# Kernel optimization log

Measured on AMD Instinct MI355X. Metric: run time of the kernel, lower is better.

The kernel has to match this reference:

```python
import jax, jax.numpy as jnp
import numpy as np

N_NODES = 100_000
N_EDGES = 1_250_000
IN_FEATS, N_HIDDEN, N_CLASSES = 64, 64, 32


def setup_inputs() -> dict:
    key = jax.random.key(0)
    ks = jax.random.split(key, 8)
    x = jax.random.normal(ks[0], (N_NODES, IN_FEATS), dtype=jnp.float32)
    src = jax.random.randint(ks[1], (N_EDGES,), 0, N_NODES, dtype=jnp.int64)
    dst = jax.random.randint(ks[2], (N_EDGES,), 0, N_NODES, dtype=jnp.int64)
    s1 = 1.0 / np.sqrt(IN_FEATS)
    s2 = 1.0 / np.sqrt(N_HIDDEN)
    W_self1 = jax.random.normal(ks[3], (IN_FEATS, N_HIDDEN), dtype=jnp.float32) * s1
    W_neigh1 = jax.random.normal(ks[4], (IN_FEATS, N_HIDDEN), dtype=jnp.float32) * s1
    b1 = jnp.zeros((N_HIDDEN,), dtype=jnp.float32)
    W_self2 = jax.random.normal(ks[5], (N_HIDDEN, N_CLASSES), dtype=jnp.float32) * s2
    W_neigh2 = jax.random.normal(ks[6], (N_HIDDEN, N_CLASSES), dtype=jnp.float32) * s2
    b2 = jnp.zeros((N_CLASSES,), dtype=jnp.float32)
    return dict(x=x, src=src, dst=dst, W_self1=W_self1, W_neigh1=W_neigh1, b1=b1,
                W_self2=W_self2, W_neigh2=W_neigh2, b2=b2)


def _sage_conv(h, src, dst, W_self, W_neigh, b):
    # mean aggregation over in-neighbors: gather src feats, segment-sum by dst
    n = h.shape[0]
    msg = h[src]  # [E, d] -- dominant memory traffic
    agg = jax.ops.segment_sum(msg, dst, num_segments=n)
    deg = jax.ops.segment_sum(jnp.ones_like(dst, dtype=h.dtype), dst, num_segments=n)
    h_neigh = agg / jnp.maximum(deg, 1.0)[:, None]  # zero-degree nodes get 0 (DGL behavior)
    return h @ W_self + h_neigh @ W_neigh + b


def reference(x, src, dst, W_self1, W_neigh1, b1, W_self2, W_neigh2, b2):
    h = _sage_conv(x, src, dst, W_self1, W_neigh1, b1)
    h = jax.nn.relu(h)
    # dropout(p=0.5) is identity in eval mode
    return _sage_conv(h, src, dst, W_self2, W_neigh2, b2)
```

## Files before the change

### kernel.cpp

```cpp
#include <hip/hip_runtime.h>
#include <hip/hip_bf16.h>


#define NF 64
#define BW 256
#define BSH 8
#define MAXB 512
#define CAPMAX 8192
#define P1_CHUNK 2048
#define H1S 68

typedef __attribute__((ext_vector_type(8))) short short8;
typedef __attribute__((ext_vector_type(8))) unsigned short ushort8v;
typedef __attribute__((ext_vector_type(4))) float floatx4;

__device__ __forceinline__ short bf16hi(float v) {
    __hip_bfloat16 h = __float2bfloat16(v);
    return *(short*)&h;
}
__device__ __forceinline__ float bf2f(short s) {
    __hip_bfloat16 h = *(__hip_bfloat16*)&s;
    return __bfloat162float(h);
}
__device__ __forceinline__ float bits2f(unsigned short u) {
    unsigned int x = ((unsigned int)u) << 16;
    union { unsigned int i; float f; } c; c.i = x; return c.f;
}


__global__ __launch_bounds__(256) void prep_kernel(
        int* __restrict__ gcursor,
        const float* __restrict__ Ws1, const float* __restrict__ Wn1,
        const float* __restrict__ Ws2, const float* __restrict__ Wn2,
        unsigned short* __restrict__ w1p, unsigned short* __restrict__ w2p) {
    const int tid = threadIdx.x;
    if (blockIdx.x == 0) {
        for (int i = tid; i < MAXB; i += 256) gcursor[i] = 0;
        return;
    }
    const int part = blockIdx.x - 1;
    for (int i = tid; i < 32 * 64; i += 256) {
        int n = part * 32 + (i >> 6), k = i & 63;
        float v = (n < 64) ? Ws1[k * 64 + n] : Wn1[k * 64 + (n - 64)];
        short hv = bf16hi(v);
        w1p[n * 64 + k] = (unsigned short)hv;
        w1p[8192 + n * 64 + k] = (unsigned short)bf16hi(v - bf2f(hv));
    }
    for (int i = tid; i < 16 * 64; i += 256) {
        int n = part * 16 + (i >> 6), k = i & 63;
        float v = (n < 32) ? Ws2[k * 32 + n] : Wn2[k * 32 + (n - 32)];
        short hv = bf16hi(v);
        w2p[n * 64 + k] = (unsigned short)hv;
        w2p[4096 + n * 64 + k] = (unsigned short)bf16hi(v - bf2f(hv));
    }
}


__global__ __launch_bounds__(256) void p1_dense1_kernel(
        const int* __restrict__ src, const int* __restrict__ dst,
        int* __restrict__ gcursor, unsigned* __restrict__ bucket,
        int E, int nbuckets, int dblocks,
        const float* __restrict__ X,
        const unsigned short* __restrict__ w1p,
        const float* __restrict__ bias,
        float* __restrict__ outA,
        unsigned short* __restrict__ outB,
        int N) {
    __shared__ int smem_i[2 * MAXB];
    const int tid = threadIdx.x;

    if ((int)blockIdx.x >= dblocks) {
        int* cnt   = smem_i;
        int* cbase = smem_i + MAXB;
        const int bid = blockIdx.x - dblocks;
        const int beg = bid * P1_CHUNK;
        const int end = min(E, beg + P1_CHUNK);
        for (int i = tid; i < nbuckets; i += 256) cnt[i] = 0;
        __syncthreads();
        for (int e = beg + tid; e < end; e += 256)
            atomicAdd(&cnt[dst[e] >> BSH], 1);
        __syncthreads();
        for (int i = tid; i < nbuckets; i += 256) {
            int c = cnt[i];
            cbase[i] = c ? atomicAdd(&gcursor[i], c) : 0;
            cnt[i] = 0;
        }
        __syncthreads();
        for (int e = beg + tid; e < end; e += 256) {
            int d = dst[e];
            int r = d >> BSH;
            int p = cbase[r] + atomicAdd(&cnt[r], 1);
            if (p < CAPMAX)
                bucket[(size_t)r * CAPMAX + p] = ((unsigned)src[e] << BSH) | (unsigned)(d & (BW - 1));
        }
        return;
    }

    constexpr int NT = 8, NSELF = 4;
    const int lane = tid & 63;
    const int wid  = tid >> 6;
    const int m = lane & 15, quad = lane >> 4;
    const int rowblk = blockIdx.x * 128 + wid * 32;

    floatx4 acc[2][NT];
    #pragma unroll
    for (int rt = 0; rt < 2; ++rt)
        #pragma unroll
        for (int t = 0; t < NT; ++t) acc[rt][t] = (floatx4)(0.f);

    short8 ah[2][2], al[2][2];
    #pragma unroll
    for (int rt = 0; rt < 2; ++rt) {
        int r = rowblk + rt * 16 + m;
        if (r >= N) r = N - 1;
        const float* xp = X + (size_t)r * 64 + quad * 8;
        #pragma unroll
        for (int h = 0; h < 2; ++h) {
            floatx4 f0 = *(const floatx4*)(xp + h * 32);
            floatx4 f1 = *(const floatx4*)(xp + h * 32 + 4);
            short8 hi, lo;
            #pragma unroll
            for (int j = 0; j < 4; ++j) {
                short hv = bf16hi(f0[j]);
                hi[j] = hv; lo[j] = bf16hi(f0[j] - bf2f(hv));
                short hv2 = bf16hi(f1[j]);
                hi[4 + j] = hv2; lo[4 + j] = bf16hi(f1[j] - bf2f(hv2));
            }
            ah[rt][h] = hi; al[rt][h] = lo;
        }
    }

    #pragma unroll
    for (int t = 0; t < NT; ++t) {
        int n = t * 16 + m;
        const unsigned short* ph = w1p + n * 64 + quad * 8;
        const unsigned short* pl = ph + 8192;
        #pragma unroll
        for (int h = 0; h < 2; ++h) {
            short8 bh = *(const short8*)(ph + h * 32);
            short8 bl = *(const short8*)(pl + h * 32);
            #pragma unroll
            for (int rt = 0; rt < 2; ++rt) {
                acc[rt][t] = __builtin_amdgcn_mfma_f32_16x16x32_bf16(ah[rt][h], bh, acc[rt][t], 0, 0, 0);
                acc[rt][t] = __builtin_amdgcn_mfma_f32_16x16x32_bf16(al[rt][h], bh, acc[rt][t], 0, 0, 0);
                acc[rt][t] = __builtin_amdgcn_mfma_f32_16x16x32_bf16(ah[rt][h], bl, acc[rt][t], 0, 0, 0);
            }
        }
    }

    #pragma unroll
    for (int rt = 0; rt < 2; ++rt) {
        #pragma unroll
        for (int t = 0; t < NT; ++t) {
            #pragma unroll
            for (int r4 = 0; r4 < 4; ++r4) {
                int row = rowblk + rt * 16 + quad * 4 + r4;
                if (row < N) {
                    if (t < NSELF) {
                        int col = t * 16 + m;
                        outA[(size_t)row * 64 + col] = acc[rt][t][r4] + bias[col];
                    } else {
                        int col = (t - NSELF) * 16 + m;
                        outB[(size_t)row * 64 + col] = (unsigned short)bf16hi(acc[rt][t][r4]);
                    }
                }
            }
        }
    }
}


__global__ __launch_bounds__(256) void p2_csr_kernel(const unsigned* __restrict__ bucket,
                                                     const int* __restrict__ gcursor,
                                                     int* __restrict__ row_start,
                                                     int* __restrict__ csr_src,
                                                     int N, int nbuckets) {
    __shared__ unsigned stage[CAPMAX];
    __shared__ int cnt[BW];
    __shared__ int excl[BW];
    const int r = blockIdx.x;
    const int tid = threadIdx.x;

    int partial = 0;
    for (int i = tid; i < r; i += 256) partial += min(gcursor[i], CAPMAX);
    excl[tid] = partial;
    __syncthreads();
    for (int off = 128; off > 0; off >>= 1) {
        if (tid < off) excl[tid] += excl[tid + off];
        __syncthreads();
    }
    const int base = excl[0];
    const int sz = min(gcursor[r], CAPMAX);
    const unsigned* bsrc = bucket + (size_t)r * CAPMAX;
    __syncthreads();

    cnt[tid] = 0;
    __syncthreads();
    for (int i = tid; i < sz; i += 256) {
        unsigned v = bsrc[i];
        stage[i] = v;
        atomicAdd(&cnt[v & (BW - 1)], 1);
    }
    __syncthreads();
    excl[tid] = cnt[tid];
    __syncthreads();
    for (int off = 1; off < BW; off <<= 1) {
        int v0 = (tid >= off) ? excl[tid - off] : 0;
        __syncthreads();
        excl[tid] += v0;
        __syncthreads();
    }
    int node = r * BW + tid;
    if (node < N) row_start[node] = base + excl[tid] - cnt[tid];
    if (r == nbuckets - 1 && tid == 0) row_start[N] = base + sz;
    __syncthreads();
    cnt[tid] = excl[tid] - cnt[tid];
    __syncthreads();
    for (int i = tid; i < sz; i += 256) {
        unsigned v = stage[i];
        int p = atomicAdd(&cnt[v & (BW - 1)], 1);
        csr_src[base + p] = (int)(v >> BSH);
    }
}


__global__ __launch_bounds__(256) void agg64_d2_kernel(
        const unsigned short* __restrict__ t1n,
        const float* __restrict__ xs,
        const int* __restrict__ row_start,
        const int* __restrict__ csr_src,
        const unsigned short* __restrict__ w2p,
        const float* __restrict__ b2,
        float* __restrict__ outD,
        unsigned short* __restrict__ t2n,
        int N, int E) {
    __shared__ float h1s[16][H1S];
    const int tid = threadIdx.x;
    const int lane = tid & 63;
    const int wid  = tid >> 6;
    const int half = lane >> 5;
    const int g = (lane >> 3) & 3;
    const int c = lane & 7;
    const int nbase = blockIdx.x * 16;

    const int ln0 = wid * 4 + half;
    const int ln1 = ln0 + 2;
    const int n0 = nbase + ln0, n1 = nbase + ln1;
    int beg0 = 0, end0 = 0, beg1 = 0, end1 = 0;
    if (n0 < N) { beg0 = row_start[n0]; end0 = row_start[n0 + 1]; }
    if (n1 < N) { beg1 = row_start[n1]; end1 = row_start[n1 + 1]; }

    float a0[8] = {0.f, 0.f, 0.f, 0.f, 0.f, 0.f, 0.f, 0.f};
    float a1[8] = {0.f, 0.f, 0.f, 0.f, 0.f, 0.f, 0.f, 0.f};
    int j0 = beg0 + g, j1 = beg1 + g;
    const int Em1 = E - 1;
    while ((j0 < end0) || (j1 < end1)) {
        int s0 = csr_src[min(j0, Em1)];
        int s1 = csr_src[min(j0 + 4, Em1)];
        int s2 = csr_src[min(j1, Em1)];
        int s3 = csr_src[min(j1 + 4, Em1)];
        s0 = ((unsigned)s0 < (unsigned)N) ? s0 : 0;
        s1 = ((unsigned)s1 < (unsigned)N) ? s1 : 0;
        s2 = ((unsigned)s2 < (unsigned)N) ? s2 : 0;
        s3 = ((unsigned)s3 < (unsigned)N) ? s3 : 0;
        ushort8v u0 = *(const ushort8v*)(t1n + (size_t)s0 * 64 + c * 8);
        ushort8v u1 = *(const ushort8v*)(t1n + (size_t)s1 * 64 + c * 8);
        ushort8v u2 = *(const ushort8v*)(t1n + (size_t)s2 * 64 + c * 8);
        ushort8v u3 = *(const ushort8v*)(t1n + (size_t)s3 * 64 + c * 8);
        const bool c00 = j0 < end0, c01 = j0 + 4 < end0;
        const bool c10 = j1 < end1, c11 = j1 + 4 < end1;
        #pragma unroll
        for (int i = 0; i < 8; ++i) {
            a0[i] += (c00 ? bits2f(u0[i]) : 0.f) + (c01 ? bits2f(u1[i]) : 0.f);
            a1[i] += (c10 ? bits2f(u2[i]) : 0.f) + (c11 ? bits2f(u3[i]) : 0.f);
        }
        j0 += 8; j1 += 8;
    }

    const int m = lane & 15, quad = lane >> 4;
    const int coln = wid * 16 + m;
    const unsigned short* pb = w2p + coln * 64 + quad * 8;
    short8 bhf0 = *(const short8*)(pb);
    short8 bhf1 = *(const short8*)(pb + 32);
    short8 blf0 = *(const short8*)(pb + 4096);
    short8 blf1 = *(const short8*)(pb + 4096 + 32);

    floatx4 x00 = (floatx4)(0.f), x01 = (floatx4)(0.f);
    floatx4 x10 = (floatx4)(0.f), x11 = (floatx4)(0.f);
    if (g == 0) {
        if (n0 < N) {
            const float* p = xs + (size_t)n0 * 64 + c * 8;
            x00 = *(const floatx4*)p; x01 = *(const floatx4*)(p + 4);
        }
        if (n1 < N) {
            const float* p = xs + (size_t)n1 * 64 + c * 8;
            x10 = *(const floatx4*)p; x11 = *(const floatx4*)(p + 4);
        }
    }

    #pragma unroll
    for (int i = 0; i < 8; ++i) {
        float v = a0[i];
        v += __shfl_xor(v, 8);
        v += __shfl_xor(v, 16);
        a0[i] = v;
        float w = a1[i];
        w += __shfl_xor(w, 8);
        w += __shfl_xor(w, 16);
        a1[i] = w;
    }
    if (g == 0) {
        floatx4 h0, h1v;
        if (n0 < N) {
            float invd = 1.0f / fmaxf((float)(end0 - beg0), 1.0f);
            #pragma unroll
            for (int i = 0; i < 4; ++i) {
                h0[i]  = fmaxf(x00[i] + a0[i] * invd, 0.f);
                h1v[i] = fmaxf(x01[i] + a0[4 + i] * invd, 0.f);
            }
        } else { h0 = (floatx4)(0.f); h1v = (floatx4)(0.f); }
        *(floatx4*)&h1s[ln0][c * 8]     = h0;
        *(floatx4*)&h1s[ln0][c * 8 + 4] = h1v;
        if (n1 < N) {
            float invd = 1.0f / fmaxf((float)(end1 - beg1), 1.0f);
            #pragma unroll
            for (int i = 0; i < 4; ++i) {
                h0[i]  = fmaxf(x10[i] + a1[i] * invd, 0.f);
                h1v[i] = fmaxf(x11[i] + a1[4 + i] * invd, 0.f);
            }
        } else { h0 = (floatx4)(0.f); h1v = (floatx4)(0.f); }
        *(floatx4*)&h1s[ln1][c * 8]     = h0;
        *(floatx4*)&h1s[ln1][c * 8 + 4] = h1v;
    }
    __syncthreads();

    short8 ah[2], al[2];
    #pragma unroll
    for (int h = 0; h < 2; ++h) {
        const float* hp = &h1s[m][quad * 8 + h * 32];
        floatx4 f0 = *(const floatx4*)hp;
        floatx4 f1 = *(const floatx4*)(hp + 4);
        short8 hi, lo;
        #pragma unroll
        for (int j = 0; j < 4; ++j) {
            short hv = bf16hi(f0[j]);
            hi[j] = hv; lo[j] = bf16hi(f0[j] - bf2f(hv));
            short hv2 = bf16hi(f1[j]);
            hi[4 + j] = hv2; lo[4 + j] = bf16hi(f1[j] - bf2f(hv2));
        }
        ah[h] = hi; al[h] = lo;
    }
    floatx4 acc2 = (floatx4)(0.f);
    acc2 = __builtin_amdgcn_mfma_f32_16x16x32_bf16(ah[0], bhf0, acc2, 0, 0, 0);
    acc2 = __builtin_amdgcn_mfma_f32_16x16x32_bf16(al[0], bhf0, acc2, 0, 0, 0);
    acc2 = __builtin_amdgcn_mfma_f32_16x16x32_bf16(ah[0], blf0, acc2, 0, 0, 0);
    acc2 = __builtin_amdgcn_mfma_f32_16x16x32_bf16(ah[1], bhf1, acc2, 0, 0, 0);
    acc2 = __builtin_amdgcn_mfma_f32_16x16x32_bf16(al[1], bhf1, acc2, 0, 0, 0);
    acc2 = __builtin_amdgcn_mfma_f32_16x16x32_bf16(ah[1], blf1, acc2, 0, 0, 0);
    #pragma unroll
    for (int r4 = 0; r4 < 4; ++r4) {
        int node = nbase + quad * 4 + r4;
        if (node < N) {
            if (coln < 32) outD[(size_t)node * 32 + coln] = acc2[r4] + b2[coln];
            else t2n[(size_t)node * 32 + (coln - 32)] = (unsigned short)bf16hi(acc2[r4]);
        }
    }
}


__global__ __launch_bounds__(256) void agg32_kernel(float* io,
                                                    const unsigned short* __restrict__ t2n,
                                                    const int* __restrict__ row_start,
                                                    const int* __restrict__ csr_src, int N) {
    int n = (blockIdx.x * blockDim.x + threadIdx.x) >> 6;
    if (n >= N) return;
    int lane = threadIdx.x & 63;
    int g = lane >> 2, c = lane & 3;
    int beg = row_start[n], end = row_start[n + 1];
    floatx4 s0v = (floatx4)(0.f), s1v = (floatx4)(0.f);
    size_t o = (size_t)n * 32 + c * 8;
    if (g == 0) {
        s0v = *(const floatx4*)(io + o);
        s1v = *(const floatx4*)(io + o + 4);
    }
    float acc[8] = {0.f, 0.f, 0.f, 0.f, 0.f, 0.f, 0.f, 0.f};
    for (int j = beg + g; j < end; j += 32) {
        int j2 = j + 16;
        int s0 = csr_src[j];
        ushort8v u0 = *(const ushort8v*)(t2n + (size_t)s0 * 32 + c * 8);
        if (j2 < end) {
            int s1 = csr_src[j2];
            ushort8v u1 = *(const ushort8v*)(t2n + (size_t)s1 * 32 + c * 8);
            #pragma unroll
            for (int i = 0; i < 8; ++i) acc[i] += bits2f(u0[i]) + bits2f(u1[i]);
        } else {
            #pragma unroll
            for (int i = 0; i < 8; ++i) acc[i] += bits2f(u0[i]);
        }
    }
    #pragma unroll
    for (int i = 0; i < 8; ++i) {
        float v = acc[i];
        v += __shfl_xor(v, 4);
        v += __shfl_xor(v, 8);
        v += __shfl_xor(v, 16);
        v += __shfl_xor(v, 32);
        acc[i] = v;
    }
    if (g == 0) {
        float inv = 1.0f / fmaxf((float)(end - beg), 1.0f);
        floatx4 r0, r1;
        #pragma unroll
        for (int i = 0; i < 4; ++i) {
            r0[i] = s0v[i] + acc[i] * inv;
            r1[i] = s1v[i] + acc[4 + i] * inv;
        }
        *(floatx4*)(io + o) = r0;
        *(floatx4*)(io + o + 4) = r1;
    }
}


__global__ __launch_bounds__(256) void deg_kernel(const int* __restrict__ dst,
                                                  float* __restrict__ deg, int E) {
    int e = blockIdx.x * blockDim.x + threadIdx.x;
    if (e < E) atomicAdd(&deg[dst[e]], 1.0f);
}

__global__ __launch_bounds__(256) void agg_atomic_kernel(const float* __restrict__ feats,
                                                         const int* __restrict__ src,
                                                         const int* __restrict__ dst,
                                                         float* __restrict__ agg, int E) {
    int tid = blockIdx.x * blockDim.x + threadIdx.x;
    if (tid >= E * NF) return;
    int e = tid >> 6, f = tid & 63;
    atomicAdd(&agg[(size_t)dst[e] * NF + f], feats[(size_t)src[e] * NF + f]);
}

__global__ __launch_bounds__(256) void layer1_fb_kernel(const float* __restrict__ x,
                                                        const float* __restrict__ agg,
                                                        const float* __restrict__ deg,
                                                        const float* __restrict__ Wself,
                                                        const float* __restrict__ Wneigh,
                                                        const float* __restrict__ b,
                                                        float* __restrict__ h1, int N) {
    int tid = blockIdx.x * blockDim.x + threadIdx.x;
    if (tid >= N * NF) return;
    int n = tid >> 6, c = tid & 63;
    float inv = 1.0f / fmaxf(deg[n], 1.0f);
    const float* xrow = x + (size_t)n * NF;
    const float* arow = agg + (size_t)n * NF;
    float acc = b[c];
    #pragma unroll
    for (int k = 0; k < NF; ++k) {
        acc += xrow[k] * Wself[k * NF + c];
        acc += (arow[k] * inv) * Wneigh[k * NF + c];
    }
    h1[tid] = fmaxf(acc, 0.f);
}

__global__ __launch_bounds__(256) void layer2_fb_kernel(const float* __restrict__ h1,
                                                        const float* __restrict__ agg,
                                                        const float* __restrict__ deg,
                                                        const float* __restrict__ Wself,
                                                        const float* __restrict__ Wneigh,
                                                        const float* __restrict__ b,
                                                        float* __restrict__ out, int N) {
    int tid = blockIdx.x * blockDim.x + threadIdx.x;
    if (tid >= N * 32) return;
    int n = tid >> 5, c = tid & 31;
    float inv = 1.0f / fmaxf(deg[n], 1.0f);
    const float* hrow = h1 + (size_t)n * NF;
    const float* arow = agg + (size_t)n * NF;
    float acc = b[c];
    #pragma unroll
    for (int k = 0; k < NF; ++k) {
        acc += hrow[k] * Wself[k * 32 + c];
        acc += (arow[k] * inv) * Wneigh[k * 32 + c];
    }
    out[tid] = acc;
}


extern "C" void kernel_launch(void* const* d_in, const int* in_sizes, int n_in,
                              void* d_out, int out_size, void* d_ws, size_t ws_size,
                              hipStream_t stream) {
    const float* x        = (const float*)d_in[0];
    const int*   src      = (const int*)d_in[1];
    const int*   dst      = (const int*)d_in[2];
    const float* W_self1  = (const float*)d_in[3];
    const float* W_neigh1 = (const float*)d_in[4];
    const float* b1       = (const float*)d_in[5];
    const float* W_self2  = (const float*)d_in[6];
    const float* W_neigh2 = (const float*)d_in[7];
    const float* b2       = (const float*)d_in[8];
    float* out = (float*)d_out;

    const int N = in_sizes[0] / NF;
    const int E = in_sizes[1];
    const int nbuckets = (N + BW - 1) / BW;

    const size_t rsPad = ((size_t)N + 8) & ~7ull;
    int* gcursor   = (int*)d_ws;
    unsigned short* w2p = (unsigned short*)(gcursor + MAXB);
    unsigned short* w1p = w2p + 8192;
    int* row_start = (int*)(w1p + 16384);
    int* csr_src   = row_start + rsPad;
    uintptr_t pa = (uintptr_t)(csr_src + (((size_t)E + 7) & ~7ull));
    pa = (pa + 127) & ~(uintptr_t)127;
    float* bufA = (float*)pa;
    unsigned* bucket = (unsigned*)bufA;
    unsigned short* t1n = (unsigned short*)(bufA + (size_t)N * NF);
    unsigned short* t2n = t1n + (size_t)N * NF;
    size_t need = (size_t)((char*)(t2n + (size_t)N * 32) - (char*)d_ws);

    bool fast = ws_size >= need
             && nbuckets <= MAXB
             && (size_t)nbuckets * CAPMAX <= (size_t)N * NF
             && (size_t)E * 2 / (size_t)nbuckets <= CAPMAX
             && N < (1 << 24)
             && out_size >= N * 32;

    if (fast) {
        prep_kernel<<<5, 256, 0, stream>>>(gcursor, W_self1, W_neigh1,
                                           W_self2, W_neigh2, w1p, w2p);
        int dblocks  = (N + 127) / 128;
        int p1blocks = (E + P1_CHUNK - 1) / P1_CHUNK;
        unsigned* bucket2 = (unsigned*)(t2n + (((size_t)N * 32 + 63) & ~63ull));
        size_t need2 = (size_t)((char*)(bucket2 + (size_t)nbuckets * CAPMAX) - (char*)d_ws);
        if (ws_size >= need2) {
            p1_dense1_kernel<<<dblocks + p1blocks, 256, 0, stream>>>(
                src, dst, gcursor, bucket2, E, nbuckets, dblocks,
                x, w1p, b1, bufA, t1n, N);
            p2_csr_kernel<<<nbuckets, 256, 0, stream>>>(bucket2, gcursor,
                                                        row_start, csr_src, N, nbuckets);
        } else {
            p1_dense1_kernel<<<p1blocks, 256, 0, stream>>>(
                src, dst, gcursor, bucket, E, nbuckets, 0,
                x, w1p, b1, bufA, t1n, N);
            p2_csr_kernel<<<nbuckets, 256, 0, stream>>>(bucket, gcursor,
                                                        row_start, csr_src, N, nbuckets);
            p1_dense1_kernel<<<dblocks, 256, 0, stream>>>(
                src, dst, gcursor, bucket, E, nbuckets, dblocks,
                x, w1p, b1, bufA, t1n, N);
        }
        agg64_d2_kernel<<<(N + 15) / 16, 256, 0, stream>>>(
            t1n, bufA, row_start, csr_src, w2p, b2, out, t2n, N, E);
        agg32_kernel<<<(N * 64 + 255) / 256, 256, 0, stream>>>(out, t2n,
                                                               row_start, csr_src, N);
    } else {
        float* deg = (float*)d_ws;
        float* agg = deg + N;
        float* h1  = agg + (size_t)N * NF;
        hipMemsetAsync(deg, 0, (size_t)(N + (size_t)N * NF) * sizeof(float), stream);
        deg_kernel<<<(E + 255) / 256, 256, 0, stream>>>(dst, deg, E);
        int at = E * NF;
        agg_atomic_kernel<<<(at + 255) / 256, 256, 0, stream>>>(x, src, dst, agg, E);
        layer1_fb_kernel<<<(N * NF + 255) / 256, 256, 0, stream>>>(x, agg, deg, W_self1,
                                                                   W_neigh1, b1, h1, N);
        hipMemsetAsync(agg, 0, (size_t)N * NF * sizeof(float), stream);
        agg_atomic_kernel<<<(at + 255) / 256, 256, 0, stream>>>(h1, src, dst, agg, E);
        layer2_fb_kernel<<<(N * 32 + 255) / 256, 256, 0, stream>>>(h1, agg, deg, W_self2,
                                                                   W_neigh2, b2, out, N);
    }
}
```

Measured before the change: 213.8 us.

## Build CSR via degree histogram, prefix scan and global-atomic scatter

Replaces the two-pass bucketed CSR construction (LDS-local bucket sort into a staging buffer, then a per-bucket counting sort) with a degree histogram using global atomics, a two-kernel prefix scan to get row_start, and a direct scatter of src ids into csr_src using per-node atomic cursors. The scatter stays fused with the first dense layer kernel. This removes the bucket staging buffer and the LDS-heavy sort kernel, but adds a memset, two scan kernels, and about a million global atomics on random addresses. Edge order within a row is no longer deterministic, which can change floating-point summation order.

```diff
diff --git a/kernel.cpp b/kernel.cpp
--- a/kernel.cpp
+++ b/kernel.cpp
@@ -3,16 +3,12 @@
 
 
 #define NF 64
-#define BW 256
-#define BSH 8
-#define MAXB 512
-#define CAPMAX 8192
-#define P1_CHUNK 2048
 #define H1S 68
 
 typedef __attribute__((ext_vector_type(8))) short short8;
 typedef __attribute__((ext_vector_type(8))) unsigned short ushort8v;
 typedef __attribute__((ext_vector_type(4))) float floatx4;
+typedef __attribute__((ext_vector_type(4))) int intx4;
 
 __device__ __forceinline__ short bf16hi(float v) {
     __hip_bfloat16 h = __float2bfloat16(v);
@@ -28,71 +24,147 @@
 }
 
 
-__global__ __launch_bounds__(256) void prep_kernel(
-        int* __restrict__ gcursor,
+__global__ __launch_bounds__(256) void pack_hist_kernel(
+        const int* __restrict__ dst, int* __restrict__ deg, int E, int N,
         const float* __restrict__ Ws1, const float* __restrict__ Wn1,
         const float* __restrict__ Ws2, const float* __restrict__ Wn2,
         unsigned short* __restrict__ w1p, unsigned short* __restrict__ w2p) {
     const int tid = threadIdx.x;
-    if (blockIdx.x == 0) {
-        for (int i = tid; i < MAXB; i += 256) gcursor[i] = 0;
+    if (blockIdx.x < 4) {
+        const int part = blockIdx.x;
+        for (int i = tid; i < 32 * 64; i += 256) {
+            int n = part * 32 + (i >> 6), k = i & 63;
+            float v = (n < 64) ? Ws1[k * 64 + n] : Wn1[k * 64 + (n - 64)];
+            short hv = bf16hi(v);
+            w1p[n * 64 + k] = (unsigned short)hv;
+            w1p[8192 + n * 64 + k] = (unsigned short)bf16hi(v - bf2f(hv));
+        }
+        for (int i = tid; i < 16 * 64; i += 256) {
+            int n = part * 16 + (i >> 6), k = i & 63;
+            float v = (n < 32) ? Ws2[k * 32 + n] : Wn2[k * 32 + (n - 32)];
+            short hv = bf16hi(v);
+            w2p[n * 64 + k] = (unsigned short)hv;
+            w2p[4096 + n * 64 + k] = (unsigned short)bf16hi(v - bf2f(hv));
+        }
         return;
     }
-    const int part = blockIdx.x - 1;
-    for (int i = tid; i < 32 * 64; i += 256) {
-        int n = part * 32 + (i >> 6), k = i & 63;
-        float v = (n < 64) ? Ws1[k * 64 + n] : Wn1[k * 64 + (n - 64)];
-        short hv = bf16hi(v);
-        w1p[n * 64 + k] = (unsigned short)hv;
-        w1p[8192 + n * 64 + k] = (unsigned short)bf16hi(v - bf2f(hv));
-    }
-    for (int i = tid; i < 16 * 64; i += 256) {
-        int n = part * 16 + (i >> 6), k = i & 63;
-        float v = (n < 32) ? Ws2[k * 32 + n] : Wn2[k * 32 + (n - 32)];
-        short hv = bf16hi(v);
-        w2p[n * 64 + k] = (unsigned short)hv;
-        w2p[4096 + n * 64 + k] = (unsigned short)bf16hi(v - bf2f(hv));
-    }
-}
-
-
-__global__ __launch_bounds__(256) void p1_dense1_kernel(
+    const int base = (blockIdx.x - 4) * 1024 + tid;
+    #pragma unroll
+    for (int k = 0; k < 4; ++k) {
+        int e = base + k * 256;
+        if (e < E) {
+            int d = dst[e];
+            if ((unsigned)d < (unsigned)N) atomicAdd(&deg[d], 1);
+        }
+    }
+}
+
+
+__global__ __launch_bounds__(256) void scan1_kernel(const int* __restrict__ deg,
+                                                    int* __restrict__ blocksum, int N) {
+    __shared__ int red[256];
+    const int t = threadIdx.x;
+    const int base = blockIdx.x * 1024;
+    int s = 0;
+    #pragma unroll
+    for (int k = 0; k < 4; ++k) {
+        int n = base + t + k * 256;
+        if (n < N) s += deg[n];
+    }
+    red[t] = s;
+    __syncthreads();
+    for (int off = 128; off > 0; off >>= 1) {
+        if (t < off) red[t] += red[t + off];
+        __syncthreads();
+    }
+    if (t == 0) blocksum[blockIdx.x] = red[0];
+}
+
+
+__global__ __launch_bounds__(256) void scan3_kernel(const int* __restrict__ deg,
+                                                    const int* __restrict__ blocksum,
+                                                    int* __restrict__ row_start,
+                                                    int* __restrict__ cursor,
+                                                    int N, int NB, int E) {
+    __shared__ int lds[256];
+    const int b = blockIdx.x, t = threadIdx.x;
+    int partial = 0;
+    for (int i = t; i < b; i += 256) partial += blocksum[i];
+    lds[t] = partial;
+    __syncthreads();
+    for (int off = 128; off > 0; off >>= 1) {
+        if (t < off) lds[t] += lds[t + off];
+        __syncthreads();
+    }
+    const int boff = lds[0];
+    __syncthreads();
+
+    const int n0 = b * 1024 + t * 4;
+    int d0 = 0, d1 = 0, d2 = 0, d3 = 0;
+    if (n0 + 3 < N) {
+        intx4 v = *(const intx4*)(deg + n0);
+        d0 = v[0]; d1 = v[1]; d2 = v[2]; d3 = v[3];
+    } else {
+        if (n0 + 0 < N) d0 = deg[n0];
+        if (n0 + 1 < N) d1 = deg[n0 + 1];
+        if (n0 + 2 < N) d2 = deg[n0 + 2];
+        if (n0 + 3 < N) d3 = deg[n0 + 3];
+    }
+    const int tsum = d0 + d1 + d2 + d3;
+    lds[t] = tsum;
+    __syncthreads();
+    for (int off = 1; off < 256; off <<= 1) {
+        int v = (t >= off) ? lds[t - off] : 0;
+        __syncthreads();
+        lds[t] += v;
+        __syncthreads();
+    }
+    const int excl = boff + lds[t] - tsum;
+    const int r0 = excl, r1 = r0 + d0, r2 = r1 + d1, r3 = r2 + d2;
+    if (n0 + 3 < N) {
+        intx4 rv; rv[0] = r0; rv[1] = r1; rv[2] = r2; rv[3] = r3;
+        *(intx4*)(row_start + n0) = rv;
+        *(intx4*)(cursor + n0) = rv;
+    } else {
+        if (n0 + 0 < N) { row_start[n0]     = r0; cursor[n0]     = r0; }
+        if (n0 + 1 < N) { row_start[n0 + 1] = r1; cursor[n0 + 1] = r1; }
+        if (n0 + 2 < N) { row_start[n0 + 2] = r2; cursor[n0 + 2] = r2; }
+        if (n0 + 3 < N) { row_start[n0 + 3] = r3; cursor[n0 + 3] = r3; }
+    }
+    if (b == NB - 1 && t == 255) row_start[N] = E;
+}
+
+
+__global__ __launch_bounds__(256) void dense1_scatter_kernel(
         const int* __restrict__ src, const int* __restrict__ dst,
-        int* __restrict__ gcursor, unsigned* __restrict__ bucket,
-        int E, int nbuckets, int dblocks,
+        int* __restrict__ cursor, int* __restrict__ csr_src,
+        int E, int dblocks,
         const float* __restrict__ X,
         const unsigned short* __restrict__ w1p,
         const float* __restrict__ bias,
         float* __restrict__ outA,
         unsigned short* __restrict__ outB,
         int N) {
-    __shared__ int smem_i[2 * MAXB];
     const int tid = threadIdx.x;
 
     if ((int)blockIdx.x >= dblocks) {
-        int* cnt   = smem_i;
-        int* cbase = smem_i + MAXB;
-        const int bid = blockIdx.x - dblocks;
-        const int beg = bid * P1_CHUNK;
-        const int end = min(E, beg + P1_CHUNK);
-        for (int i = tid; i < nbuckets; i += 256) cnt[i] = 0;
-        __syncthreads();
-        for (int e = beg + tid; e < end; e += 256)
-            atomicAdd(&cnt[dst[e] >> BSH], 1);
-        __syncthreads();
-        for (int i = tid; i < nbuckets; i += 256) {
-            int c = cnt[i];
-            cbase[i] = c ? atomicAdd(&gcursor[i], c) : 0;
-            cnt[i] = 0;
-        }
-        __syncthreads();
-        for (int e = beg + tid; e < end; e += 256) {
-            int d = dst[e];
-            int r = d >> BSH;
-            int p = cbase[r] + atomicAdd(&cnt[r], 1);
-            if (p < CAPMAX)
-                bucket[(size_t)r * CAPMAX + p] = ((unsigned)src[e] << BSH) | (unsigned)(d & (BW - 1));
-        }
+        const int base = (blockIdx.x - dblocks) * 1024 + tid;
+        const int e0 = base, e1 = base + 256, e2 = base + 512, e3 = base + 768;
+        int d0 = 0, d1 = 0, d2 = 0, d3 = 0, s0 = 0, s1 = 0, s2 = 0, s3 = 0;
+        const bool v0 = e0 < E, v1 = e1 < E, v2 = e2 < E, v3 = e3 < E;
+        if (v0) { d0 = dst[e0]; s0 = src[e0]; }
+        if (v1) { d1 = dst[e1]; s1 = src[e1]; }
+        if (v2) { d2 = dst[e2]; s2 = src[e2]; }
+        if (v3) { d3 = dst[e3]; s3 = src[e3]; }
+        int p0 = 0, p1 = 0, p2 = 0, p3 = 0;
+        if (v0 && (unsigned)d0 < (unsigned)N) p0 = atomicAdd(&cursor[d0], 1); else p0 = -1;
+        if (v1 && (unsigned)d1 < (unsigned)N) p1 = atomicAdd(&cursor[d1], 1); else p1 = -1;
+        if (v2 && (unsigned)d2 < (unsigned)N) p2 = atomicAdd(&cursor[d2], 1); else p2 = -1;
+        if (v3 && (unsigned)d3 < (unsigned)N) p3 = atomicAdd(&cursor[d3], 1); else p3 = -1;
+        if (p0 >= 0) csr_src[p0] = s0;
+        if (p1 >= 0) csr_src[p1] = s1;
+        if (p2 >= 0) csr_src[p2] = s2;
+        if (p3 >= 0) csr_src[p3] = s3;
         return;
     }
 
@@ -166,60 +238,6 @@
                 }
             }
         }
-    }
-}
-
-
-__global__ __launch_bounds__(256) void p2_csr_kernel(const unsigned* __restrict__ bucket,
-                                                     const int* __restrict__ gcursor,
-                                                     int* __restrict__ row_start,
-                                                     int* __restrict__ csr_src,
-                                                     int N, int nbuckets) {
-    __shared__ unsigned stage[CAPMAX];
-    __shared__ int cnt[BW];
-    __shared__ int excl[BW];
-    const int r = blockIdx.x;
-    const int tid = threadIdx.x;
-
-    int partial = 0;
-    for (int i = tid; i < r; i += 256) partial += min(gcursor[i], CAPMAX);
-    excl[tid] = partial;
-    __syncthreads();
-    for (int off = 128; off > 0; off >>= 1) {
-        if (tid < off) excl[tid] += excl[tid + off];
-        __syncthreads();
-    }
-    const int base = excl[0];
-    const int sz = min(gcursor[r], CAPMAX);
-    const unsigned* bsrc = bucket + (size_t)r * CAPMAX;
-    __syncthreads();
-
-    cnt[tid] = 0;
-    __syncthreads();
-    for (int i = tid; i < sz; i += 256) {
-        unsigned v = bsrc[i];
-        stage[i] = v;
-        atomicAdd(&cnt[v & (BW - 1)], 1);
-    }
-    __syncthreads();
-    excl[tid] = cnt[tid];
-    __syncthreads();
-    for (int off = 1; off < BW; off <<= 1) {
-        int v0 = (tid >= off) ? excl[tid - off] : 0;
-        __syncthreads();
-        excl[tid] += v0;
-        __syncthreads();
-    }
-    int node = r * BW + tid;
-    if (node < N) row_start[node] = base + excl[tid] - cnt[tid];
-    if (r == nbuckets - 1 && tid == 0) row_start[N] = base + sz;
-    __syncthreads();
-    cnt[tid] = excl[tid] - cnt[tid];
-    __syncthreads();
-    for (int i = tid; i < sz; i += 256) {
-        unsigned v = stage[i];
-        int p = atomicAdd(&cnt[v & (BW - 1)], 1);
-        csr_src[base + p] = (int)(v >> BSH);
     }
 }
 
@@ -498,69 +516,55 @@
 
     const int N = in_sizes[0] / NF;
     const int E = in_sizes[1];
-    const int nbuckets = (N + BW - 1) / BW;
-
-    const size_t rsPad = ((size_t)N + 8) & ~7ull;
-    int* gcursor   = (int*)d_ws;
-    unsigned short* w2p = (unsigned short*)(gcursor + MAXB);
-    unsigned short* w1p = w2p + 8192;
-    int* row_start = (int*)(w1p + 16384);
-    int* csr_src   = row_start + rsPad;
-    uintptr_t pa = (uintptr_t)(csr_src + (((size_t)E + 7) & ~7ull));
-    pa = (pa + 127) & ~(uintptr_t)127;
-    float* bufA = (float*)pa;
-    unsigned* bucket = (unsigned*)bufA;
-    unsigned short* t1n = (unsigned short*)(bufA + (size_t)N * NF);
-    unsigned short* t2n = t1n + (size_t)N * NF;
-    size_t need = (size_t)((char*)(t2n + (size_t)N * 32) - (char*)d_ws);
+    const int NB = (N + 1023) / 1024;
+
+    uintptr_t p = (uintptr_t)d_ws;
+    auto align_up = [](uintptr_t v, uintptr_t a) { return (v + a - 1) & ~(a - 1); };
+    int* deg = (int*)p;            p += (size_t)N * 4;       p = align_up(p, 64);
+    int* cursor = (int*)p;         p += (size_t)N * 4;       p = align_up(p, 64);
+    int* row_start = (int*)p;      p += ((size_t)N + 8) * 4; p = align_up(p, 64);
+    int* blocksum = (int*)p;       p += 1024;                p = align_up(p, 64);
+    unsigned short* w2p = (unsigned short*)p; p += 8192 * 2;
+    unsigned short* w1p = (unsigned short*)p; p += 16384 * 2;
+    int* csr_src = (int*)p;        p += (size_t)E * 4;       p = align_up(p, 128);
+    float* bufA = (float*)p;       p += (size_t)N * 64 * 4;
+    unsigned short* t1n = (unsigned short*)p; p += (size_t)N * 64 * 2;
+    unsigned short* t2n = (unsigned short*)p; p += (size_t)N * 32 * 2;
+    size_t need = (size_t)(p - (uintptr_t)d_ws);
 
     bool fast = ws_size >= need
-             && nbuckets <= MAXB
-             && (size_t)nbuckets * CAPMAX <= (size_t)N * NF
-             && (size_t)E * 2 / (size_t)nbuckets <= CAPMAX
-             && N < (1 << 24)
+             && NB <= 256
+             && N >= 4
              && out_size >= N * 32;
 
     if (fast) {
-        prep_kernel<<<5, 256, 0, stream>>>(gcursor, W_self1, W_neigh1,
-                                           W_self2, W_neigh2, w1p, w2p);
-        int dblocks  = (N + 127) / 128;
-        int p1blocks = (E + P1_CHUNK - 1) / P1_CHUNK;
-        unsigned* bucket2 = (unsigned*)(t2n + (((size_t)N * 32 + 63) & ~63ull));
-        size_t need2 = (size_t)((char*)(bucket2 + (size_t)nbuckets * CAPMAX) - (char*)d_ws);
-        if (ws_size >= need2) {
-            p1_dense1_kernel<<<dblocks + p1blocks, 256, 0, stream>>>(
-                src, dst, gcursor, bucket2, E, nbuckets, dblocks,
-                x, w1p, b1, bufA, t1n, N);
-            p2_csr_kernel<<<nbuckets, 256, 0, stream>>>(bucket2, gcursor,
-                                                        row_start, csr_src, N, nbuckets);
-        } else {
-            p1_dense1_kernel<<<p1blocks, 256, 0, stream>>>(
-                src, dst, gcursor, bucket, E, nbuckets, 0,
-                x, w1p, b1, bufA, t1n, N);
-            p2_csr_kernel<<<nbuckets, 256, 0, stream>>>(bucket, gcursor,
-                                                        row_start, csr_src, N, nbuckets);
-            p1_dense1_kernel<<<dblocks, 256, 0, stream>>>(
-                src, dst, gcursor, bucket, E, nbuckets, dblocks,
-                x, w1p, b1, bufA, t1n, N);
-        }
+        const int hblocks = (E + 1023) / 1024;
+        const int dblocks = (N + 127) / 128;
+        hipMemsetAsync(deg, 0, (size_t)N * sizeof(int), stream);
+        pack_hist_kernel<<<4 + hblocks, 256, 0, stream>>>(
+            dst, deg, E, N, W_self1, W_neigh1, W_self2, W_neigh2, w1p, w2p);
+        scan1_kernel<<<NB, 256, 0, stream>>>(deg, blocksum, N);
+        scan3_kernel<<<NB, 256, 0, stream>>>(deg, blocksum, row_start, cursor, N, NB, E);
+        dense1_scatter_kernel<<<dblocks + hblocks, 256, 0, stream>>>(
+            src, dst, cursor, csr_src, E, dblocks,
+            x, w1p, b1, bufA, t1n, N);
         agg64_d2_kernel<<<(N + 15) / 16, 256, 0, stream>>>(
             t1n, bufA, row_start, csr_src, w2p, b2, out, t2n, N, E);
         agg32_kernel<<<(N * 64 + 255) / 256, 256, 0, stream>>>(out, t2n,
                                                                row_start, csr_src, N);
     } else {
-        float* deg = (float*)d_ws;
-        float* agg = deg + N;
+        float* deg_f = (float*)d_ws;
+        float* agg = deg_f + N;
         float* h1  = agg + (size_t)N * NF;
-        hipMemsetAsync(deg, 0, (size_t)(N + (size_t)N * NF) * sizeof(float), stream);
-        deg_kernel<<<(E + 255) / 256, 256, 0, stream>>>(dst, deg, E);
+        hipMemsetAsync(deg_f, 0, (size_t)(N + (size_t)N * NF) * sizeof(float), stream);
+        deg_kernel<<<(E + 255) / 256, 256, 0, stream>>>(dst, deg_f, E);
         int at = E * NF;
         agg_atomic_kernel<<<(at + 255) / 256, 256, 0, stream>>>(x, src, dst, agg, E);
-        layer1_fb_kernel<<<(N * NF + 255) / 256, 256, 0, stream>>>(x, agg, deg, W_self1,
+        layer1_fb_kernel<<<(N * NF + 255) / 256, 256, 0, stream>>>(x, agg, deg_f, W_self1,
                                                                    W_neigh1, b1, h1, N);
         hipMemsetAsync(agg, 0, (size_t)N * NF * sizeof(float), stream);
         agg_atomic_kernel<<<(at + 255) / 256, 256, 0, stream>>>(h1, src, dst, agg, E);
-        layer2_fb_kernel<<<(N * 32 + 255) / 256, 256, 0, stream>>>(h1, agg, deg, W_self2,
+        layer2_fb_kernel<<<(N * 32 + 255) / 256, 256, 0, stream>>>(h1, agg, deg_f, W_self2,
                                                                    W_neigh2, b2, out, N);
     }
 }
```

After: 311.8 us. 45.8% more time.

## Prefetch next CSR indices in agg64 and pack four nodes per wave in agg32

Applied to the files above, without the earlier changes.

In the layer-1 aggregation loop, the next iteration's csr_src indices are loaded ahead, while the current feature gathers are in flight. This hides index-load latency. The layer-2 aggregation kernel now assigns 16 lanes per node instead of a full 64-lane wave, so each wave handles four nodes. That cuts idle lanes for nodes with around 12 neighbours and shortens the shuffle reduction. It adds clamped, possibly redundant index loads and needs E>0, which is now checked.

```diff
diff --git a/kernel.cpp b/kernel.cpp
--- a/kernel.cpp
+++ b/kernel.cpp
@@ -254,19 +254,23 @@
     float a1[8] = {0.f, 0.f, 0.f, 0.f, 0.f, 0.f, 0.f, 0.f};
     int j0 = beg0 + g, j1 = beg1 + g;
     const int Em1 = E - 1;
+    int i0 = csr_src[min(j0, Em1)];
+    int i1 = csr_src[min(j0 + 4, Em1)];
+    int i2 = csr_src[min(j1, Em1)];
+    int i3 = csr_src[min(j1 + 4, Em1)];
     while ((j0 < end0) || (j1 < end1)) {
-        int s0 = csr_src[min(j0, Em1)];
-        int s1 = csr_src[min(j0 + 4, Em1)];
-        int s2 = csr_src[min(j1, Em1)];
-        int s3 = csr_src[min(j1 + 4, Em1)];
-        s0 = ((unsigned)s0 < (unsigned)N) ? s0 : 0;
-        s1 = ((unsigned)s1 < (unsigned)N) ? s1 : 0;
-        s2 = ((unsigned)s2 < (unsigned)N) ? s2 : 0;
-        s3 = ((unsigned)s3 < (unsigned)N) ? s3 : 0;
+        int s0 = ((unsigned)i0 < (unsigned)N) ? i0 : 0;
+        int s1 = ((unsigned)i1 < (unsigned)N) ? i1 : 0;
+        int s2 = ((unsigned)i2 < (unsigned)N) ? i2 : 0;
+        int s3 = ((unsigned)i3 < (unsigned)N) ? i3 : 0;
         ushort8v u0 = *(const ushort8v*)(t1n + (size_t)s0 * 64 + c * 8);
         ushort8v u1 = *(const ushort8v*)(t1n + (size_t)s1 * 64 + c * 8);
         ushort8v u2 = *(const ushort8v*)(t1n + (size_t)s2 * 64 + c * 8);
         ushort8v u3 = *(const ushort8v*)(t1n + (size_t)s3 * 64 + c * 8);
+        i0 = csr_src[min(j0 + 8, Em1)];
+        i1 = csr_src[min(j0 + 12, Em1)];
+        i2 = csr_src[min(j1 + 8, Em1)];
+        i3 = csr_src[min(j1 + 12, Em1)];
         const bool c00 = j0 < end0, c01 = j0 + 4 < end0;
         const bool c10 = j1 < end1, c11 = j1 + 4 < end1;
         #pragma unroll
@@ -371,43 +375,49 @@
 __global__ __launch_bounds__(256) void agg32_kernel(float* io,
                                                     const unsigned short* __restrict__ t2n,
                                                     const int* __restrict__ row_start,
-                                                    const int* __restrict__ csr_src, int N) {
-    int n = (blockIdx.x * blockDim.x + threadIdx.x) >> 6;
-    if (n >= N) return;
-    int lane = threadIdx.x & 63;
-    int g = lane >> 2, c = lane & 3;
-    int beg = row_start[n], end = row_start[n + 1];
+                                                    const int* __restrict__ csr_src,
+                                                    int N, int E) {
+    const int tid = threadIdx.x;
+    const int lane = tid & 63;
+    const int wid = tid >> 6;
+    const int slot = lane >> 4;
+    const int g = (lane >> 2) & 3;
+    const int c = lane & 3;
+    const int n = blockIdx.x * 16 + wid * 4 + slot;
+
+    int beg = 0, end = 0;
+    if (n < N) { beg = row_start[n]; end = row_start[n + 1]; }
+
     floatx4 s0v = (floatx4)(0.f), s1v = (floatx4)(0.f);
     size_t o = (size_t)n * 32 + c * 8;
-    if (g == 0) {
+    if (n < N && g == 0) {
         s0v = *(const floatx4*)(io + o);
         s1v = *(const floatx4*)(io + o + 4);
     }
+
     float acc[8] = {0.f, 0.f, 0.f, 0.f, 0.f, 0.f, 0.f, 0.f};
-    for (int j = beg + g; j < end; j += 32) {
-        int j2 = j + 16;
+    const int Em1 = E - 1;
+    for (int j = beg + g; j < end; j += 8) {
+        int j2 = j + 4;
         int s0 = csr_src[j];
+        int s1 = csr_src[min(j2, Em1)];
+        s0 = ((unsigned)s0 < (unsigned)N) ? s0 : 0;
+        s1 = ((unsigned)s1 < (unsigned)N) ? s1 : 0;
         ushort8v u0 = *(const ushort8v*)(t2n + (size_t)s0 * 32 + c * 8);
-        if (j2 < end) {
-            int s1 = csr_src[j2];
-            ushort8v u1 = *(const ushort8v*)(t2n + (size_t)s1 * 32 + c * 8);
-            #pragma unroll
-            for (int i = 0; i < 8; ++i) acc[i] += bits2f(u0[i]) + bits2f(u1[i]);
-        } else {
-            #pragma unroll
-            for (int i = 0; i < 8; ++i) acc[i] += bits2f(u0[i]);
-        }
+        ushort8v u1 = *(const ushort8v*)(t2n + (size_t)s1 * 32 + c * 8);
+        const bool c1 = j2 < end;
+        #pragma unroll
+        for (int i = 0; i < 8; ++i)
+            acc[i] += bits2f(u0[i]) + (c1 ? bits2f(u1[i]) : 0.f);
     }
     #pragma unroll
     for (int i = 0; i < 8; ++i) {
         float v = acc[i];
         v += __shfl_xor(v, 4);
         v += __shfl_xor(v, 8);
-        v += __shfl_xor(v, 16);
-        v += __shfl_xor(v, 32);
         acc[i] = v;
     }
-    if (g == 0) {
+    if (n < N && g == 0) {
         float inv = 1.0f / fmaxf((float)(end - beg), 1.0f);
         floatx4 r0, r1;
         #pragma unroll
@@ -515,6 +525,7 @@
     size_t need = (size_t)((char*)(t2n + (size_t)N * 32) - (char*)d_ws);
 
     bool fast = ws_size >= need
+             && E > 0
              && nbuckets <= MAXB
              && (size_t)nbuckets * CAPMAX <= (size_t)N * NF
              && (size_t)E * 2 / (size_t)nbuckets <= CAPMAX
@@ -546,8 +557,8 @@
         }
         agg64_d2_kernel<<<(N + 15) / 16, 256, 0, stream>>>(
             t1n, bufA, row_start, csr_src, w2p, b2, out, t2n, N, E);
-        agg32_kernel<<<(N * 64 + 255) / 256, 256, 0, stream>>>(out, t2n,
-                                                               row_start, csr_src, N);
+        agg32_kernel<<<(N + 15) / 16, 256, 0, stream>>>(out, t2n,
+                                                        row_start, csr_src, N, E);
     } else {
         float* deg = (float*)d_ws;
         float* agg = deg + N;
```

New measurement: 203.6 us. -4.8%, faster.
